# Kernel tuning notes

Measured on AMD Instinct MI355X. Metric: run time of the kernel, lower is better.

## Reference

```python
import jax, jax.numpy as jnp
import numpy as np

TEMPERATURE = 0.5
B, D = 4096, 256

def setup_inputs() -> dict:
    key = jax.random.key(0)
    k1, k2 = jax.random.split(key)
    z_i = jax.random.normal(k1, (B, D), dtype=jnp.float32)
    z_j = jax.random.normal(k2, (B, D), dtype=jnp.float32)
    return {"z_i": z_i, "z_j": z_j}

def reference(z_i, z_j):
    # NT-Xent loss (SimCLR). Cosine similarity of L2-normalized rows == dot product.
    b = z_i.shape[0]
    n = 2 * b
    zi = z_i / jnp.linalg.norm(z_i, axis=1, keepdims=True)
    zj = z_j / jnp.linalg.norm(z_j, axis=1, keepdims=True)
    z = jnp.concatenate([zi, zj], axis=0)            # [N, D]
    sim = jnp.matmul(z, z.T)                          # [N, N] cosine-sim matrix
    # positives: sim(i, i+b) and sim(i+b, i)
    pos = jnp.concatenate([jnp.diagonal(sim, offset=b), jnp.diagonal(sim, offset=-b)])  # [N]
    logits = sim / TEMPERATURE
    # Cross-entropy with the positive as the target class over {pos} U negatives.
    # The candidate set per row is all j != i (the positive j = partner(i) is included,
    # only the self-similarity diagonal is excluded) -> mask diagonal with -inf.
    neg_inf = jnp.asarray(-jnp.inf, dtype=logits.dtype)
    masked = jnp.where(jnp.eye(n, dtype=bool), neg_inf, logits)
    lse = jax.nn.logsumexp(masked, axis=1)            # [N]
    loss = jnp.sum(lse - pos / TEMPERATURE) / n
    return loss
```

## Files before the change

kernel.cpp:

```cpp
#include <hip/hip_runtime.h>
#include <hip/hip_bf16.h>


constexpr int BB = 4096;
constexpr int NN = 8192;
constexpr int DD = 256;
constexpr int RT = 256;
constexpr int CC = 512;
constexpr int NRT = NN / RT;
constexpr int NCH = NN / CC;
constexpr int CSTEPS = CC / 32;

typedef _Float16 half4v __attribute__((ext_vector_type(4)));
typedef _Float16 half8v __attribute__((ext_vector_type(8)));
typedef float floatx16 __attribute__((ext_vector_type(16)));

#define SQK 1.69864414f

__global__ __launch_bounds__(256) void nt_normalize(
    const float* __restrict__ zi, const float* __restrict__ zj,
    _Float16* __restrict__ Z, float* __restrict__ posPartial,
    float* __restrict__ rowsum)
{
    const int lane = threadIdx.x & 63;
    const int wave = threadIdx.x >> 6;
    const int i = blockIdx.x * 4 + wave;

    if (blockIdx.x < 32) rowsum[blockIdx.x * 256 + threadIdx.x] = 0.f;

    const float4 a = ((const float4*)(zi + (size_t)i * DD))[lane];
    const float4 b = ((const float4*)(zj + (size_t)i * DD))[lane];

    float ssi = a.x*a.x + a.y*a.y + a.z*a.z + a.w*a.w;
    float ssj = b.x*b.x + b.y*b.y + b.z*b.z + b.w*b.w;
    float dd  = a.x*b.x + a.y*b.y + a.z*b.z + a.w*b.w;
#pragma unroll
    for (int off = 32; off > 0; off >>= 1) {
        ssi += __shfl_xor(ssi, off);
        ssj += __shfl_xor(ssj, off);
        dd  += __shfl_xor(dd,  off);
    }
    const float invi = rsqrtf(ssi) * SQK;
    const float invj = rsqrtf(ssj) * SQK;

    half4v ha, hb;
    ha.x = (_Float16)(a.x * invi); ha.y = (_Float16)(a.y * invi);
    ha.z = (_Float16)(a.z * invi); ha.w = (_Float16)(a.w * invi);
    hb.x = (_Float16)(b.x * invj); hb.y = (_Float16)(b.y * invj);
    hb.z = (_Float16)(b.z * invj); hb.w = (_Float16)(b.w * invj);

    ((half4v*)(Z + (size_t)i * DD))[lane]        = ha;
    ((half4v*)(Z + (size_t)(BB + i) * DD))[lane] = hb;

    __shared__ float ps[4];
    if (lane == 0) ps[wave] = dd * invi * invj * (1.0f / (SQK * SQK));
    __syncthreads();
    if (threadIdx.x == 0)
        posPartial[blockIdx.x] = ps[0] + ps[1] + ps[2] + ps[3];
}

__global__ __launch_bounds__(256, 2) void nt_simexp(
    const _Float16* __restrict__ Z, float* __restrict__ rowsum)
{
    __shared__ _Float16 lds[2][32 * DD];

    const int bid = blockIdx.x;
    const int rt = bid & (NRT - 1);
    const int ch = bid >> 5;
    const int tid = threadIdx.x;
    const int wave = tid >> 6;
    const int lane = tid & 63;
    const int lm = lane & 31;
    const int lh = lane >> 5;

    const int rbase = rt * RT + wave * 64;

    half8v bfrag[2][16];
#pragma unroll
    for (int b = 0; b < 2; ++b) {
        const _Float16* rowp = Z + (size_t)(rbase + b * 32 + lm) * DD + lh * 8;
#pragma unroll
        for (int s = 0; s < 16; ++s)
            bfrag[b][s] = *(const half8v*)(rowp + s * 16);
    }

    const int g_c0 = tid >> 5;
    const int g_kc = tid & 31;
    const int cchunk = ch * CC;

    half8v pre[4];
    auto loadTile = [&](int cs) {
#pragma unroll
        for (int it = 0; it < 4; ++it) {
            const int c = g_c0 + it * 8;
            pre[it] = *(const half8v*)(Z + (size_t)(cchunk + cs * 32 + c) * DD + g_kc * 8);
        }
    };
    auto storeTile = [&](int buf) {
#pragma unroll
        for (int it = 0; it < 4; ++it) {
            const int c = g_c0 + it * 8;
            *(half8v*)(&lds[buf][c * DD + (g_kc ^ (c & 7)) * 8]) = pre[it];
        }
    };

    float ea0 = 0.f, ea1 = 0.f, eb0 = 0.f, eb1 = 0.f;
    const bool blockdiag = (ch == (rt >> 1));

    loadTile(0);
    storeTile(0);

    for (int cs = 0; cs < CSTEPS; ++cs) {
        const int cbase = cchunk + cs * 32;

        __syncthreads();
        if (cs + 1 < CSTEPS) loadTile(cs + 1);

        floatx16 c0, c1;
#pragma unroll
        for (int r = 0; r < 16; ++r) { c0[r] = 0.f; c1[r] = 0.f; }

        const _Float16* abuf = lds[cs & 1];
#pragma unroll
        for (int s = 0; s < 16; ++s) {
            const int phys = (2 * s + lh) ^ (lm & 7);
            half8v af = *(const half8v*)(&abuf[lm * DD + phys * 8]);
            c0 = __builtin_amdgcn_mfma_f32_32x32x16_f16(af, bfrag[0][s], c0, 0, 0, 0);
            c1 = __builtin_amdgcn_mfma_f32_32x32x16_f16(af, bfrag[1][s], c1, 0, 0, 0);
        }

        const bool m0 = blockdiag && (cbase == rbase);
        const bool m1 = blockdiag && (cbase == rbase + 32);
        if (!(m0 | m1)) {
#pragma unroll
            for (int r = 0; r < 16; r += 2) {
                ea0 += __builtin_amdgcn_exp2f(c0[r]);
                eb0 += __builtin_amdgcn_exp2f(c0[r + 1]);
                ea1 += __builtin_amdgcn_exp2f(c1[r]);
                eb1 += __builtin_amdgcn_exp2f(c1[r + 1]);
            }
        } else {
#pragma unroll
            for (int r = 0; r < 16; ++r) {
                const int mrow = (r & 3) + 8 * (r >> 2) + 4 * lh;
                float e0 = __builtin_amdgcn_exp2f(c0[r]);
                float e1 = __builtin_amdgcn_exp2f(c1[r]);
                if (m0 && (mrow == lm)) e0 = 0.f;
                if (m1 && (mrow == lm)) e1 = 0.f;
                if (r & 1) { eb0 += e0; eb1 += e1; }
                else       { ea0 += e0; ea1 += e1; }
            }
        }

        if (cs + 1 < CSTEPS) storeTile((cs + 1) & 1);
    }

    ea0 += eb0; ea1 += eb1;
    ea0 += __shfl_xor(ea0, 32);
    ea1 += __shfl_xor(ea1, 32);
    if (lane < 32) {
        atomicAdd(&rowsum[rbase + lm], ea0);
        atomicAdd(&rowsum[rbase + 32 + lm], ea1);
    }
}

__global__ __launch_bounds__(256) void nt_finalize(
    const float* __restrict__ rowsum, const float* __restrict__ posPartial,
    float* __restrict__ out)
{
    const int tid = threadIdx.x;
    float acc = 0.f;
#pragma unroll
    for (int it = 0; it < NN / 256; ++it)
        acc += __builtin_amdgcn_logf(rowsum[tid + it * 256]);
    float pacc = 0.f;
#pragma unroll
    for (int it = 0; it < 4; ++it)
        pacc += posPartial[tid + it * 256];

#pragma unroll
    for (int off = 32; off > 0; off >>= 1) {
        acc  += __shfl_xor(acc,  off);
        pacc += __shfl_xor(pacc, off);
    }
    __shared__ float sa[4], sp[4];
    const int wave = tid >> 6;
    if ((tid & 63) == 0) { sa[wave] = acc; sp[wave] = pacc; }
    __syncthreads();
    if (tid == 0) {
        const float lntot = (sa[0] + sa[1] + sa[2] + sa[3]) * 0.6931471805599453f;
        const float ptot  = sp[0] + sp[1] + sp[2] + sp[3];
        out[0] = (lntot - 4.0f * ptot) * (1.0f / (float)NN);
    }
}

extern "C" void kernel_launch(void* const* d_in, const int* in_sizes, int n_in,
                              void* d_out, int out_size, void* d_ws, size_t ws_size,
                              hipStream_t stream) {
    const float* zi = (const float*)d_in[0];
    const float* zj = (const float*)d_in[1];
    float* out = (float*)d_out;

    _Float16* Z = (_Float16*)d_ws;
    float* rowsum = (float*)((char*)d_ws + (size_t)NN * DD * 2);
    float* posPartial = rowsum + NN;

    nt_normalize<<<BB / 4, 256, 0, stream>>>(zi, zj, Z, posPartial, rowsum);
    nt_simexp<<<NRT * NCH, 256, 0, stream>>>((const _Float16*)Z, rowsum);
    nt_finalize<<<1, 256, 0, stream>>>(rowsum, posPartial, out);
}
```

Before: 98.00 us.

## Software-pipeline MFMA tiles with the exp epilogue using double accumulators

Restructures the column-step loop so the exp2 and masking epilogue of step cs-1 runs after the MFMA chain of step cs has been issued. It alternates between two sets of accumulator registers, which lets the transcendental work overlap the matrix-core latency. The tile load, store and barrier are reordered so only one __syncthreads is needed per step. In exchange it doubles accumulator register usage, and if the loop is not fully unrolled the runtime index into the accumulator array could spill to scratch.

```diff
diff --git a/kernel.cpp b/kernel.cpp
--- a/kernel.cpp
+++ b/kernel.cpp
@@ -74,6 +74,8 @@
     const int lh = lane >> 5;
 
     const int rbase = rt * RT + wave * 64;
+    const int cchunk = ch * CC;
+    const bool blockdiag = (ch == (rt >> 1));
 
     half8v bfrag[2][16];
 #pragma unroll
@@ -86,7 +88,6 @@
 
     const int g_c0 = tid >> 5;
     const int g_kc = tid & 31;
-    const int cchunk = ch * CC;
 
     half8v pre[4];
     auto loadTile = [&](int cs) {
@@ -104,56 +105,61 @@
         }
     };
 
+    floatx16 a0[2], a1[2];
     float ea0 = 0.f, ea1 = 0.f, eb0 = 0.f, eb1 = 0.f;
-    const bool blockdiag = (ch == (rt >> 1));
-
-    loadTile(0);
-    storeTile(0);
-
-    for (int cs = 0; cs < CSTEPS; ++cs) {
-        const int cbase = cchunk + cs * 32;
-
-        __syncthreads();
-        if (cs + 1 < CSTEPS) loadTile(cs + 1);
-
-        floatx16 c0, c1;
-#pragma unroll
-        for (int r = 0; r < 16; ++r) { c0[r] = 0.f; c1[r] = 0.f; }
-
-        const _Float16* abuf = lds[cs & 1];
+
+    auto kloop = [&](int p, int buf) {
+#pragma unroll
+        for (int r = 0; r < 16; ++r) { a0[p][r] = 0.f; a1[p][r] = 0.f; }
+        const _Float16* abuf = lds[buf];
 #pragma unroll
         for (int s = 0; s < 16; ++s) {
             const int phys = (2 * s + lh) ^ (lm & 7);
             half8v af = *(const half8v*)(&abuf[lm * DD + phys * 8]);
-            c0 = __builtin_amdgcn_mfma_f32_32x32x16_f16(af, bfrag[0][s], c0, 0, 0, 0);
-            c1 = __builtin_amdgcn_mfma_f32_32x32x16_f16(af, bfrag[1][s], c1, 0, 0, 0);
-        }
-
+            a0[p] = __builtin_amdgcn_mfma_f32_32x32x16_f16(af, bfrag[0][s], a0[p], 0, 0, 0);
+            a1[p] = __builtin_amdgcn_mfma_f32_32x32x16_f16(af, bfrag[1][s], a1[p], 0, 0, 0);
+        }
+    };
+
+    auto epilogue = [&](int p, int cs) {
+        const int cbase = cchunk + cs * 32;
         const bool m0 = blockdiag && (cbase == rbase);
         const bool m1 = blockdiag && (cbase == rbase + 32);
         if (!(m0 | m1)) {
 #pragma unroll
             for (int r = 0; r < 16; r += 2) {
-                ea0 += __builtin_amdgcn_exp2f(c0[r]);
-                eb0 += __builtin_amdgcn_exp2f(c0[r + 1]);
-                ea1 += __builtin_amdgcn_exp2f(c1[r]);
-                eb1 += __builtin_amdgcn_exp2f(c1[r + 1]);
+                ea0 += __builtin_amdgcn_exp2f(a0[p][r]);
+                eb0 += __builtin_amdgcn_exp2f(a0[p][r + 1]);
+                ea1 += __builtin_amdgcn_exp2f(a1[p][r]);
+                eb1 += __builtin_amdgcn_exp2f(a1[p][r + 1]);
             }
         } else {
 #pragma unroll
             for (int r = 0; r < 16; ++r) {
                 const int mrow = (r & 3) + 8 * (r >> 2) + 4 * lh;
-                float e0 = __builtin_amdgcn_exp2f(c0[r]);
-                float e1 = __builtin_amdgcn_exp2f(c1[r]);
+                float e0 = __builtin_amdgcn_exp2f(a0[p][r]);
+                float e1 = __builtin_amdgcn_exp2f(a1[p][r]);
                 if (m0 && (mrow == lm)) e0 = 0.f;
                 if (m1 && (mrow == lm)) e1 = 0.f;
                 if (r & 1) { eb0 += e0; eb1 += e1; }
                 else       { ea0 += e0; ea1 += e1; }
             }
         }
-
-        if (cs + 1 < CSTEPS) storeTile((cs + 1) & 1);
-    }
+    };
+
+    loadTile(0);
+    storeTile(0);
+    __syncthreads();
+    kloop(0, 0);
+
+    for (int cs = 1; cs < CSTEPS; ++cs) {
+        loadTile(cs);
+        epilogue((cs - 1) & 1, cs - 1);
+        storeTile(cs & 1);
+        __syncthreads();
+        kloop(cs & 1, cs & 1);
+    }
+    epilogue((CSTEPS - 1) & 1, CSTEPS - 1);
 
     ea0 += eb0; ea1 += eb1;
     ea0 += __shfl_xor(ea0, 32);
```

After: 110.6 us. 1.13x slower.

## Exploit similarity-matrix symmetry by computing only upper-triangular tile pairs

Applied to the files above, without the earlier changes.

Launches only upper-triangular (row-tile, column-tile) pairs, mapping each block index to a tile pair with a triangular-index solve. For off-diagonal tiles, each exp value is added both to its row sum and, through a cross-lane shuffle reduction plus LDS atomics, to a per-block column sum. The column sums are flushed to the global row sums at the end, since the matrix is symmetric. This roughly halves the MFMA and exp work. In exchange it adds many shuffles, shared-memory atomics and an extra global atomic pass per block.

```diff
diff --git a/kernel.cpp b/kernel.cpp
--- a/kernel.cpp
+++ b/kernel.cpp
@@ -6,10 +6,9 @@
 constexpr int NN = 8192;
 constexpr int DD = 256;
 constexpr int RT = 256;
-constexpr int CC = 512;
-constexpr int NRT = NN / RT;
-constexpr int NCH = NN / CC;
-constexpr int CSTEPS = CC / 32;
+constexpr int NBT = NN / RT;
+constexpr int NBLK = NBT * (NBT + 1) / 2;
+constexpr int CSTEPS = RT / 32;
 
 typedef _Float16 half4v __attribute__((ext_vector_type(4)));
 typedef _Float16 half8v __attribute__((ext_vector_type(8)));
@@ -63,17 +62,23 @@
     const _Float16* __restrict__ Z, float* __restrict__ rowsum)
 {
     __shared__ _Float16 lds[2][32 * DD];
-
-    const int bid = blockIdx.x;
-    const int rt = bid & (NRT - 1);
-    const int ch = bid >> 5;
+    __shared__ float rowacc[RT];
+
+    const int t = blockIdx.x;
+    int j = (int)((sqrtf(8.0f * (float)t + 1.0f) - 1.0f) * 0.5f);
+    while ((j + 1) * (j + 2) / 2 <= t) ++j;
+    while (j * (j + 1) / 2 > t) --j;
+    const int i = t - ((j * (j + 1)) >> 1);
+    const bool blockdiag = (i == j);
+
     const int tid = threadIdx.x;
     const int wave = tid >> 6;
     const int lane = tid & 63;
     const int lm = lane & 31;
     const int lh = lane >> 5;
 
-    const int rbase = rt * RT + wave * 64;
+    const int rbase = i * RT + wave * 64;
+    const int cchunk = j * RT;
 
     half8v bfrag[2][16];
 #pragma unroll
@@ -86,7 +91,6 @@
 
     const int g_c0 = tid >> 5;
     const int g_kc = tid & 31;
-    const int cchunk = ch * CC;
 
     half8v pre[4];
     auto loadTile = [&](int cs) {
@@ -105,8 +109,8 @@
     };
 
     float ea0 = 0.f, ea1 = 0.f, eb0 = 0.f, eb1 = 0.f;
-    const bool blockdiag = (ch == (rt >> 1));
-
+
+    rowacc[tid] = 0.f;
     loadTile(0);
     storeTile(0);
 
@@ -129,15 +133,27 @@
             c1 = __builtin_amdgcn_mfma_f32_32x32x16_f16(af, bfrag[1][s], c1, 0, 0, 0);
         }
 
-        const bool m0 = blockdiag && (cbase == rbase);
-        const bool m1 = blockdiag && (cbase == rbase + 32);
-        if (!(m0 | m1)) {
-#pragma unroll
-            for (int r = 0; r < 16; r += 2) {
-                ea0 += __builtin_amdgcn_exp2f(c0[r]);
-                eb0 += __builtin_amdgcn_exp2f(c0[r + 1]);
-                ea1 += __builtin_amdgcn_exp2f(c1[r]);
-                eb1 += __builtin_amdgcn_exp2f(c1[r + 1]);
+        if (!blockdiag) {
+            float v[16];
+#pragma unroll
+            for (int r = 0; r < 16; ++r) {
+                const float e0 = __builtin_amdgcn_exp2f(c0[r]);
+                const float e1 = __builtin_amdgcn_exp2f(c1[r]);
+                if (r & 1) { eb0 += e0; eb1 += e1; }
+                else       { ea0 += e0; ea1 += e1; }
+                v[r] = e0 + e1;
+            }
+#pragma unroll
+            for (int off = 1; off <= 16; off <<= 1)
+#pragma unroll
+                for (int r = 0; r < 16; ++r)
+                    v[r] += __shfl_xor(v[r], off);
+            if (lm == 0) {
+#pragma unroll
+                for (int r = 0; r < 16; ++r) {
+                    const int mrow = (r & 3) + 8 * (r >> 2) + 4 * lh;
+                    atomicAdd(&rowacc[cs * 32 + mrow], v[r]);
+                }
             }
         } else {
 #pragma unroll
@@ -145,8 +161,8 @@
                 const int mrow = (r & 3) + 8 * (r >> 2) + 4 * lh;
                 float e0 = __builtin_amdgcn_exp2f(c0[r]);
                 float e1 = __builtin_amdgcn_exp2f(c1[r]);
-                if (m0 && (mrow == lm)) e0 = 0.f;
-                if (m1 && (mrow == lm)) e1 = 0.f;
+                if ((cbase == rbase)      && (mrow == lm)) e0 = 0.f;
+                if ((cbase == rbase + 32) && (mrow == lm)) e1 = 0.f;
                 if (r & 1) { eb0 += e0; eb1 += e1; }
                 else       { ea0 += e0; ea1 += e1; }
             }
@@ -162,6 +178,9 @@
         atomicAdd(&rowsum[rbase + lm], ea0);
         atomicAdd(&rowsum[rbase + 32 + lm], ea1);
     }
+
+    __syncthreads();
+    if (!blockdiag) atomicAdd(&rowsum[cchunk + tid], rowacc[tid]);
 }
 
 __global__ __launch_bounds__(256) void nt_finalize(
@@ -206,6 +225,6 @@
     float* posPartial = rowsum + NN;
 
     nt_normalize<<<BB / 4, 256, 0, stream>>>(zi, zj, Z, posPartial, rowsum);
-    nt_simexp<<<NRT * NCH, 256, 0, stream>>>((const _Float16*)Z, rowsum);
+    nt_simexp<<<NBLK, 256, 0, stream>>>((const _Float16*)Z, rowsum);
     nt_finalize<<<1, 256, 0, stream>>>(rowsum, posPartial, out);
 }
```

Result: slower. 105.7 us (+7.8%).
